# Kernel tuning notes

Hardware: AMD Instinct MI355X
Metric: run time of the kernel (lower is better)

## Reference

```python
import jax, jax.numpy as jnp
import numpy as np

EPS = 1e-5  # torch InstanceNorm2d default eps

def conv1x1(x, w, b):
    # x: [B,C,H,W], w: [O,C], b: [O]
    return jnp.einsum('bchw,oc->bohw', x, w) + b[None, :, None, None]

def instance_norm(x):
    # InstanceNorm2d(affine=False): normalize per-sample, per-channel over H,W
    mean = jnp.mean(x, axis=(2, 3), keepdims=True)
    var = jnp.var(x, axis=(2, 3), keepdims=True)
    return (x - mean) * jax.lax.rsqrt(var + EPS)

def proj(x, w, b):
    return jax.nn.relu(instance_norm(conv1x1(x, w, b)))

def setup_inputs() -> dict:
    key = jax.random.key(0)
    ks = jax.random.split(key, 9)
    B, C, Ci, H, W = 16, 256, 128, 64, 64
    s_in = 1.0 / np.sqrt(C)
    s_mid = 1.0 / np.sqrt(Ci)
    return {
        'x': jax.random.normal(ks[0], (B, C, H, W), jnp.float32),
        'g_w': jax.random.normal(ks[1], (Ci, C), jnp.float32) * s_in,
        'g_b': jax.random.normal(ks[2], (Ci,), jnp.float32) * s_in,
        'theta_w': jax.random.normal(ks[3], (Ci, C), jnp.float32) * s_in,
        'theta_b': jax.random.normal(ks[4], (Ci,), jnp.float32) * s_in,
        'phi_w': jax.random.normal(ks[5], (Ci, C), jnp.float32) * s_in,
        'phi_b': jax.random.normal(ks[6], (Ci,), jnp.float32) * s_in,
        'W_w': jax.random.normal(ks[7], (C, Ci), jnp.float32) * s_mid,
        'W_b': jax.random.normal(ks[8], (C,), jnp.float32) * s_mid,
    }

def reference(x, g_w, g_b, theta_w, theta_b, phi_w, phi_b, W_w, W_b):
    B, C, H, W = x.shape
    Ci = g_w.shape[0]
    N = H * W
    g_x = proj(x, g_w, g_b).reshape(B, Ci, N)        # [B,Ci,N]
    theta_x = proj(x, theta_w, theta_b).reshape(B, Ci, N)
    phi_x = proj(x, phi_w, phi_b).reshape(B, Ci, N)
    # channel-attention Gram matrix [B,Ci,Ci], softmax over last dim
    f = jnp.einsum('bin,bjn->bij', theta_x, phi_x)
    attn = jax.nn.softmax(f, axis=2)
    y = jnp.einsum('bij,bjn->bin', attn, g_x)        # [B,Ci,N]
    # replicate torch permute(0,2,1).contiguous().view(B,Ci,H,W)
    y = jnp.transpose(y, (0, 2, 1)).reshape(B, Ci, H, W)
    y = instance_norm(conv1x1(y, W_w, W_b))
    return y + x
```

## Files before the change

### kernel.cpp

```cpp
#include <hip/hip_runtime.h>

#define DEVINL __device__ __forceinline__

typedef __attribute__((ext_vector_type(8))) _Float16 h8v;
typedef __attribute__((ext_vector_type(4))) float f32x4;
typedef __attribute__((ext_vector_type(8))) unsigned short us8;
typedef __attribute__((ext_vector_type(4))) unsigned short us4;

DEVINL unsigned short f2h(float f) {
  return __builtin_bit_cast(unsigned short, (_Float16)f);
}
DEVINL float h2f(unsigned short u) {
  return (float)__builtin_bit_cast(_Float16, u);
}

__global__ __launch_bounds__(256)
void prep_weights(const float* __restrict__ g_w, const float* __restrict__ th_w,
                  const float* __restrict__ ph_w, const float* __restrict__ W_w,
                  unsigned short* __restrict__ wall_h, unsigned short* __restrict__ wall_l,
                  unsigned short* __restrict__ w2h)
{
  const int i = blockIdx.x * 256 + threadIdx.x;
  float v;
  if (i < 32768) v = th_w[i];
  else if (i < 65536) v = ph_w[i - 32768];
  else v = g_w[i - 65536];
  const unsigned short h = f2h(v);
  wall_h[i] = h;
  if (i < 65536) wall_l[i] = f2h(v - h2f(h));
  if (i < 32768) w2h[i] = f2h(W_w[i]);
}

__global__ __launch_bounds__(512, 2)
void proj_gemm(const unsigned short* __restrict__ wall_h,
               const unsigned short* __restrict__ wall_l,
               const float* __restrict__ x,
               unsigned short* __restrict__ zh, unsigned short* __restrict__ zl,
               float* __restrict__ partials)
{
  __shared__ __align__(16) unsigned short smem[64512];
  unsigned short* As_h = smem;
  unsigned short* As_l = smem + 27648;
  unsigned short* Bs_h = smem + 46080;
  unsigned short* Bs_l = smem + 55296;

  const int t = threadIdx.x;
  const int lane = t & 63;
  const int wave = t >> 6;
  const int wm = wave >> 1, wn = wave & 1;
  const int lr = lane & 15, lk = lane >> 4;
  const int b = blockIdx.z;
  const int bx = blockIdx.x;
  const int nbase = bx * 128;
  const float* xs = x + (long)b * 256 * 4096;

  f32x4 acc[6][4];
#pragma unroll
  for (int i = 0; i < 6; ++i)
#pragma unroll
    for (int j = 0; j < 4; ++j) acc[i][j] = (f32x4)0.0f;

  const int nl = t & 127, cg = t >> 7;

  for (int kt = 0; kt < 4; ++kt) {
    const int k0 = kt * 64;
#pragma unroll
    for (int i = 0; i < 6; ++i) {
      const int q = i * 512 + t;
      const int row = q >> 3, c = q & 7;
      *(us8*)&As_h[row * 72 + c * 8] = *(const us8*)&wall_h[(long)row * 256 + k0 + c * 8];
    }
#pragma unroll
    for (int i = 0; i < 4; ++i) {
      const int q = i * 512 + t;
      const int row = q >> 3, c = q & 7;
      *(us8*)&As_l[row * 72 + c * 8] = *(const us8*)&wall_l[(long)row * 256 + k0 + c * 8];
    }
#pragma unroll
    for (int hp = 0; hp < 2; ++hp) {
      float xv[8];
#pragma unroll
      for (int i = 0; i < 8; ++i)
        xv[i] = xs[(long)(k0 + cg * 16 + hp * 8 + i) * 4096 + nbase + nl];
      us8 h8, l8;
#pragma unroll
      for (int e = 0; e < 8; ++e) {
        const unsigned short hb = f2h(xv[e]);
        h8[e] = hb;
        l8[e] = f2h(xv[e] - h2f(hb));
      }
      *(us8*)&Bs_h[nl * 72 + cg * 16 + hp * 8] = h8;
      *(us8*)&Bs_l[nl * 72 + cg * 16 + hp * 8] = l8;
    }
    __syncthreads();

#pragma unroll
    for (int ks = 0; ks < 2; ++ks) {
      const int ko = ks * 32 + lk * 8;
      h8v bh[4], bl[4];
#pragma unroll
      for (int ni = 0; ni < 4; ++ni) {
        const int r = (wn * 64 + ni * 16 + lr) * 72 + ko;
        bh[ni] = *(const h8v*)&Bs_h[r];
        bl[ni] = *(const h8v*)&Bs_l[r];
      }
#pragma unroll
      for (int mi = 0; mi < 6; ++mi) {
        const int fr = mi * 4 + wm;
        const h8v ah = *(const h8v*)&As_h[(fr * 16 + lr) * 72 + ko];
        if (fr < 16) {
          const h8v al = *(const h8v*)&As_l[(fr * 16 + lr) * 72 + ko];
#pragma unroll
          for (int ni = 0; ni < 4; ++ni) {
            acc[mi][ni] = __builtin_amdgcn_mfma_f32_16x16x32_f16(bh[ni], ah, acc[mi][ni], 0, 0, 0);
            acc[mi][ni] = __builtin_amdgcn_mfma_f32_16x16x32_f16(bl[ni], ah, acc[mi][ni], 0, 0, 0);
            acc[mi][ni] = __builtin_amdgcn_mfma_f32_16x16x32_f16(bh[ni], al, acc[mi][ni], 0, 0, 0);
          }
        } else {
#pragma unroll
          for (int ni = 0; ni < 4; ++ni)
            acc[mi][ni] = __builtin_amdgcn_mfma_f32_16x16x32_f16(bh[ni], ah, acc[mi][ni], 0, 0, 0);
        }
      }
    }
    __syncthreads();
  }

  float* sbuf = (float*)smem;
  unsigned short* T = smem + 12288;
#pragma unroll
  for (int mi = 0; mi < 6; ++mi) {
    float s = 0.f, ss = 0.f;
#pragma unroll
    for (int ni = 0; ni < 4; ++ni)
#pragma unroll
      for (int r = 0; r < 4; ++r) {
        const float v = acc[mi][ni][r];
        s += v; ss += v * v;
      }
    const int fr = mi * 4 + wm;
    const int slot = ((fr * 16 + lr) * 8 + (wn * 4 + lk)) * 2;
    sbuf[slot] = s; sbuf[slot + 1] = ss;
  }
  __syncthreads();
  if (t < 384) {
    float s = 0.f, ss = 0.f;
#pragma unroll
    for (int w = 0; w < 8; ++w) {
      s += sbuf[(t * 8 + w) * 2];
      ss += sbuf[(t * 8 + w) * 2 + 1];
    }
    const long pidx = ((long)bx * 6144 + b * 384 + t) * 2;
    partials[pidx] = s; partials[pidx + 1] = ss;
  }
#pragma unroll
  for (int mi = 0; mi < 6; ++mi)
#pragma unroll
    for (int ni = 0; ni < 4; ++ni) {
      const int gm = (mi * 4 + wm) * 16 + lr;
      const int gn = wn * 64 + ni * 16 + lk * 4;
      us4 hv;
#pragma unroll
      for (int r = 0; r < 4; ++r) hv[r] = f2h(acc[mi][ni][r]);
      *(us4*)&T[gm * 132 + gn] = hv;
    }
  __syncthreads();
#pragma unroll
  for (int i = 0; i < 12; ++i) {
    const int q = i * 512 + t;
    const int row = q >> 4, c = q & 15;
    const us8 v = *(const us8*)&T[row * 132 + c * 8];
    *(us8*)&zh[((long)b * 384 + row) * 4096 + nbase + c * 8] = v;
  }
  __syncthreads();
#pragma unroll
  for (int mi = 0; mi < 4; ++mi)
#pragma unroll
    for (int ni = 0; ni < 4; ++ni) {
      const int gm = (mi * 4 + wm) * 16 + lr;
      const int gn = wn * 64 + ni * 16 + lk * 4;
      us4 lv;
#pragma unroll
      for (int r = 0; r < 4; ++r) {
        const float v = acc[mi][ni][r];
        lv[r] = f2h(v - h2f(f2h(v)));
      }
      *(us4*)&T[gm * 132 + gn] = lv;
    }
  __syncthreads();
#pragma unroll
  for (int i = 0; i < 8; ++i) {
    const int q = i * 512 + t;
    const int row = q >> 4, c = q & 15;
    const us8 v = *(const us8*)&T[row * 132 + c * 8];
    *(us8*)&zl[((long)b * 256 + row) * 4096 + nbase + c * 8] = v;
  }
}

__global__ __launch_bounds__(256)
void stats_reduce(const float* __restrict__ partials, float* __restrict__ stats)
{
  const int row = blockIdx.x * 256 + threadIdx.x;
  float s = 0.f, ss = 0.f;
#pragma unroll
  for (int k = 0; k < 32; ++k) {
    s += partials[((long)k * 6144 + row) * 2];
    ss += partials[((long)k * 6144 + row) * 2 + 1];
  }
  const float mean = s * (1.f / 4096.f);
  const float var = ss * (1.f / 4096.f) - mean * mean;
  const float rs = rsqrtf(fmaxf(var, 0.f) + 1e-5f);
  stats[row * 2] = rs;
  stats[row * 2 + 1] = -mean * rs;
}

__global__ __launch_bounds__(256, 2)
void fgemm_norm(const unsigned short* __restrict__ zh, const unsigned short* __restrict__ zl,
                const float* __restrict__ stats, float* __restrict__ fpart)
{
  __shared__ __align__(16) unsigned short As_h[128 * 72];
  __shared__ __align__(16) unsigned short As_l[128 * 72];
  __shared__ __align__(16) unsigned short Bs_h[128 * 72];
  __shared__ __align__(16) unsigned short Bs_l[128 * 72];

  const int t = threadIdx.x;
  const int lane = t & 63;
  const int wave = t >> 6;
  const int wm = wave >> 1, wn = wave & 1;
  const int lr = lane & 15, lk = lane >> 4;
  const int zb = blockIdx.z >> 5, z1 = blockIdx.z & 31;
  const int koff = z1 * 128;

  f32x4 acc[4][4];
#pragma unroll
  for (int i = 0; i < 4; ++i)
#pragma unroll
    for (int j = 0; j < 4; ++j) acc[i][j] = (f32x4)0.0f;

  for (int kt = 0; kt < 2; ++kt) {
    const int k0 = koff + kt * 64;
#pragma unroll
    for (int i = 0; i < 4; ++i) {
      const int q = i * 256 + t;
      const int row = q >> 3, c = q & 7;
#pragma unroll
      for (int op = 0; op < 2; ++op) {
        const int zrow = op * 128 + row;
        const us8 h = *(const us8*)&zh[((long)zb * 384 + zrow) * 4096 + k0 + c * 8];
        const us8 l = *(const us8*)&zl[((long)zb * 256 + zrow) * 4096 + k0 + c * 8];
        const int srow = zb * 384 + zrow;
        const float rs = stats[srow * 2];
        const float nmrs = stats[srow * 2 + 1];
        us8 oh, ol;
#pragma unroll
        for (int e = 0; e < 8; ++e) {
          const float v = h2f(h[e]) + h2f(l[e]);
          const float nv = fmaxf(__builtin_fmaf(v, rs, nmrs), 0.f);
          const unsigned short hb = f2h(nv);
          oh[e] = hb;
          ol[e] = f2h(nv - h2f(hb));
        }
        unsigned short* dh = op ? Bs_h : As_h;
        unsigned short* dl = op ? Bs_l : As_l;
        *(us8*)&dh[row * 72 + c * 8] = oh;
        *(us8*)&dl[row * 72 + c * 8] = ol;
      }
    }
    __syncthreads();
#pragma unroll
    for (int ks = 0; ks < 2; ++ks) {
      const int ko = ks * 32 + lk * 8;
      h8v ah[4], bh[4], al[4], bl[4];
#pragma unroll
      for (int mi = 0; mi < 4; ++mi) {
        const int r = (wm * 64 + mi * 16 + lr) * 72 + ko;
        ah[mi] = *(const h8v*)&As_h[r];
        al[mi] = *(const h8v*)&As_l[r];
      }
#pragma unroll
      for (int ni = 0; ni < 4; ++ni) {
        const int r = (wn * 64 + ni * 16 + lr) * 72 + ko;
        bh[ni] = *(const h8v*)&Bs_h[r];
        bl[ni] = *(const h8v*)&Bs_l[r];
      }
#pragma unroll
      for (int mi = 0; mi < 4; ++mi)
#pragma unroll
        for (int ni = 0; ni < 4; ++ni) {
          acc[mi][ni] = __builtin_amdgcn_mfma_f32_16x16x32_f16(bh[ni], ah[mi], acc[mi][ni], 0, 0, 0);
          acc[mi][ni] = __builtin_amdgcn_mfma_f32_16x16x32_f16(bl[ni], ah[mi], acc[mi][ni], 0, 0, 0);
          acc[mi][ni] = __builtin_amdgcn_mfma_f32_16x16x32_f16(bh[ni], al[mi], acc[mi][ni], 0, 0, 0);
        }
    }
    __syncthreads();
  }

  const long cOff = ((long)zb * 32 + z1) * 16384;
#pragma unroll
  for (int mi = 0; mi < 4; ++mi)
#pragma unroll
    for (int ni = 0; ni < 4; ++ni) {
      const int gm = wm * 64 + mi * 16 + lr;
      const int gn = wn * 64 + ni * 16 + lk * 4;
      *(f32x4*)&fpart[cOff + (long)gm * 128 + gn] = acc[mi][ni];
    }
}

__global__ __launch_bounds__(256, 2)
void gemm_y(const unsigned short* __restrict__ Ah0, const unsigned short* __restrict__ Bh0,
            unsigned short* __restrict__ Cout,
            int lda, int ldb, int ldc, int ksteps, int z1count,
            long aS1, long aS2, long bS1, long bS2, long cS1, long cS2)
{
  __shared__ __align__(16) unsigned short smem[18432];
  unsigned short* As = smem;
  unsigned short* Bs = smem + 9216;

  const int t = threadIdx.x;
  const int lane = t & 63;
  const int wave = t >> 6;
  const int wm = wave >> 1, wn = wave & 1;
  const int lr = lane & 15, lk = lane >> 4;

  const int z = blockIdx.z;
  const int zb = z / z1count, z1 = z - zb * z1count;
  const unsigned short* Ah = Ah0 + zb * aS2 + z1 * aS1;
  const unsigned short* Bh = Bh0 + zb * bS2 + z1 * bS1;
  const long cOff = zb * cS2 + z1 * cS1;

  f32x4 acc[4][4];
#pragma unroll
  for (int i = 0; i < 4; ++i)
#pragma unroll
    for (int j = 0; j < 4; ++j) acc[i][j] = (f32x4)0.0f;

  for (int kt = 0; kt < ksteps; ++kt) {
    const int k0 = kt * 64;
#pragma unroll
    for (int i = 0; i < 4; ++i) {
      const int q = i * 256 + t;
      const int row = q >> 3, c = q & 7;
      const int lo = row * 72 + c * 8;
      *(us8*)&As[lo] = *(const us8*)&Ah[(long)row * lda + k0 + c * 8];
      *(us8*)&Bs[lo] = *(const us8*)&Bh[(long)row * ldb + k0 + c * 8];
    }
    __syncthreads();
#pragma unroll
    for (int ks = 0; ks < 2; ++ks) {
      const int ko = ks * 32 + lk * 8;
      h8v ah[4], bh[4];
#pragma unroll
      for (int mi = 0; mi < 4; ++mi)
        ah[mi] = *(const h8v*)&As[(wm * 64 + mi * 16 + lr) * 72 + ko];
#pragma unroll
      for (int ni = 0; ni < 4; ++ni)
        bh[ni] = *(const h8v*)&Bs[(wn * 64 + ni * 16 + lr) * 72 + ko];
#pragma unroll
      for (int mi = 0; mi < 4; ++mi)
#pragma unroll
        for (int ni = 0; ni < 4; ++ni)
          acc[mi][ni] = __builtin_amdgcn_mfma_f32_16x16x32_f16(bh[ni], ah[mi], acc[mi][ni], 0, 0, 0);
    }
    __syncthreads();
  }

  unsigned short* T = smem;
#pragma unroll
  for (int mi = 0; mi < 4; ++mi)
#pragma unroll
    for (int ni = 0; ni < 4; ++ni) {
      const int gm = wm * 64 + mi * 16 + lr;
      const int gn = wn * 64 + ni * 16 + lk * 4;
      us4 o;
#pragma unroll
      for (int r = 0; r < 4; ++r) o[r] = f2h(acc[mi][ni][r]);
      *(us4*)&T[gm * 132 + gn] = o;
    }
  __syncthreads();
#pragma unroll
  for (int i = 0; i < 8; ++i) {
    const int q = i * 256 + t;
    const int row = q >> 4, c = q & 15;
    const us8 v = *(const us8*)&T[row * 132 + c * 8];
    *(us8*)&Cout[cOff + (long)row * ldc + c * 8] = v;
  }
}

__global__ __launch_bounds__(256, 2)
void conv2_gemm(const unsigned short* __restrict__ w2h,
                const unsigned short* __restrict__ y4T,
                unsigned short* __restrict__ z2b)
{
  __shared__ __align__(16) unsigned short smem[33792];
  unsigned short* As = smem;
  unsigned short* Bs = smem + 18432;

  const int t = threadIdx.x;
  const int lane = t & 63;
  const int wave = t >> 6;
  const int wm = wave >> 1, wn = wave & 1;
  const int lr = lane & 15, lk = lane >> 4;
  const int b = blockIdx.z;
  const int nbase = blockIdx.x * 128;
  const unsigned short* Bh = y4T + (long)b * 4096 * 128 + (long)nbase * 128;

  f32x4 acc[8][4];
#pragma unroll
  for (int i = 0; i < 8; ++i)
#pragma unroll
    for (int j = 0; j < 4; ++j) acc[i][j] = (f32x4)0.0f;

  for (int kt = 0; kt < 2; ++kt) {
    const int k0 = kt * 64;
#pragma unroll
    for (int i = 0; i < 8; ++i) {
      const int q = i * 256 + t;
      const int row = q >> 3, c = q & 7;
      *(us8*)&As[row * 72 + c * 8] = *(const us8*)&w2h[(long)row * 128 + k0 + c * 8];
    }
#pragma unroll
    for (int i = 0; i < 4; ++i) {
      const int q = i * 256 + t;
      const int row = q >> 3, c = q & 7;
      *(us8*)&Bs[row * 72 + c * 8] = *(const us8*)&Bh[(long)row * 128 + k0 + c * 8];
    }
    __syncthreads();
#pragma unroll
    for (int ks = 0; ks < 2; ++ks) {
      const int ko = ks * 32 + lk * 8;
      h8v ah[8], bh[4];
#pragma unroll
      for (int mi = 0; mi < 8; ++mi)
        ah[mi] = *(const h8v*)&As[(wm * 128 + mi * 16 + lr) * 72 + ko];
#pragma unroll
      for (int ni = 0; ni < 4; ++ni)
        bh[ni] = *(const h8v*)&Bs[(wn * 64 + ni * 16 + lr) * 72 + ko];
#pragma unroll
      for (int mi = 0; mi < 8; ++mi)
#pragma unroll
        for (int ni = 0; ni < 4; ++ni)
          acc[mi][ni] = __builtin_amdgcn_mfma_f32_16x16x32_f16(bh[ni], ah[mi], acc[mi][ni], 0, 0, 0);
    }
    __syncthreads();
  }

  unsigned short* T = smem;
#pragma unroll
  for (int mi = 0; mi < 8; ++mi)
#pragma unroll
    for (int ni = 0; ni < 4; ++ni) {
      const int gm = wm * 128 + mi * 16 + lr;
      const int gn = wn * 64 + ni * 16 + lk * 4;
      us4 o;
#pragma unroll
      for (int r = 0; r < 4; ++r) o[r] = f2h(acc[mi][ni][r]);
      *(us4*)&T[gm * 132 + gn] = o;
    }
  __syncthreads();
#pragma unroll
  for (int i = 0; i < 16; ++i) {
    const int q = i * 256 + t;
    const int row = q >> 4, c = q & 15;
    const us8 v = *(const us8*)&T[row * 132 + c * 8];
    *(us8*)&z2b[((long)b * 256 + row) * 4096 + nbase + c * 8] = v;
  }
}

__global__ __launch_bounds__(256)
void norm_transpose_g(const unsigned short* __restrict__ zh,
                      const float* __restrict__ stats,
                      unsigned short* __restrict__ gT)
{
  __shared__ unsigned short T[64 * 136];
  const int b = blockIdx.y, n0 = blockIdx.x * 64;
  const int t = threadIdx.x;
  const int c = t >> 1, part = t & 1;
  const int grow = b * 384 + 256 + c;
  const float rs = stats[grow * 2];
  const float nmrs = stats[grow * 2 + 1];
  const long off = (long)grow * 4096 + n0 + part * 32;
#pragma unroll
  for (int j = 0; j < 4; ++j) {
    const us8 h = *(const us8*)&zh[off + j * 8];
#pragma unroll
    for (int e = 0; e < 8; ++e) {
      const float nv = fmaxf(__builtin_fmaf(h2f(h[e]), rs, nmrs), 0.f);
      T[(part * 32 + j * 8 + e) * 136 + c] = f2h(nv);
    }
  }
  __syncthreads();
  const int nl = t >> 2, q = t & 3;
  const long obase = ((long)b * 4096 + n0 + nl) * 128 + q * 32;
#pragma unroll
  for (int k = 0; k < 4; ++k) {
    us8 o;
#pragma unroll
    for (int e = 0; e < 8; ++e) o[e] = T[nl * 136 + q * 32 + k * 8 + e];
    *(us8*)&gT[obase + k * 8] = o;
  }
}

__global__ __launch_bounds__(64)
void softmax_attn(const float* __restrict__ fpart, unsigned short* __restrict__ attn)
{
  const int row = blockIdx.x;
  const int b = row >> 7, i = row & 127;
  const int t = threadIdx.x;
  float v0 = 0.f, v1 = 0.f;
#pragma unroll
  for (int kc = 0; kc < 32; ++kc) {
    const float* p = fpart + ((long)(b * 32 + kc)) * 16384 + i * 128;
    v0 += p[t];
    v1 += p[t + 64];
  }
  float mx = fmaxf(v0, v1);
  for (int o = 32; o > 0; o >>= 1) mx = fmaxf(mx, __shfl_xor(mx, o));
  const float e0 = __expf(v0 - mx), e1 = __expf(v1 - mx);
  float s = e0 + e1;
  for (int o = 32; o > 0; o >>= 1) s += __shfl_xor(s, o);
  const float inv = 1.f / s;
  attn[(long)row * 128 + t] = f2h(e0 * inv);
  attn[(long)row * 128 + t + 64] = f2h(e1 * inv);
}

__global__ __launch_bounds__(256)
void finalize(const unsigned short* __restrict__ z2b, const float* __restrict__ x,
              float* __restrict__ out)
{
  const int row = blockIdx.x;
  const long base = (long)row * 4096;
  const int t = threadIdx.x;
  float v[16];
  float s = 0.f, ss = 0.f;
#pragma unroll
  for (int h = 0; h < 2; ++h) {
    us8 u = *(const us8*)&z2b[base + t * 16 + h * 8];
#pragma unroll
    for (int e = 0; e < 8; ++e) {
      const float f = h2f(u[e]);
      v[h * 8 + e] = f;
      s += f; ss += f * f;
    }
  }
  __shared__ float r0[256], r1[256];
  r0[t] = s; r1[t] = ss;
  __syncthreads();
  for (int o = 128; o > 0; o >>= 1) {
    if (t < o) { r0[t] += r0[t + o]; r1[t] += r1[t + o]; }
    __syncthreads();
  }
  const float mean = r0[0] * (1.f / 4096.f);
  const float var = r1[0] * (1.f / 4096.f) - mean * mean;
  const float rs = rsqrtf(fmaxf(var, 0.f) + 1e-5f);
#pragma unroll
  for (int i = 0; i < 4; ++i) {
    f32x4 xr = *(const f32x4*)&x[base + t * 16 + i * 4];
    f32x4 o;
#pragma unroll
    for (int e = 0; e < 4; ++e) o[e] = (v[i * 4 + e] - mean) * rs + xr[e];
    *(f32x4*)&out[base + t * 16 + i * 4] = o;
  }
}

extern "C" void kernel_launch(void* const* d_in, const int* in_sizes, int n_in,
                              void* d_out, int out_size, void* d_ws, size_t ws_size,
                              hipStream_t stream)
{
  const float* x    = (const float*)d_in[0];
  const float* g_w  = (const float*)d_in[1];
  const float* th_w = (const float*)d_in[3];
  const float* ph_w = (const float*)d_in[5];
  const float* W_w  = (const float*)d_in[7];

  char* ws = (char*)d_ws;
  const size_t MB = 1024ull * 1024ull;
  if (ws_size < 186 * MB) return;

  unsigned short* zh       = (unsigned short*)(ws);
  unsigned short* zl       = (unsigned short*)(ws + 51 * MB);
  float*          fpart    = (float*)(ws + 85 * MB);
  unsigned short* attn     = (unsigned short*)(ws + 119 * MB);
  unsigned short* gT       = (unsigned short*)(ws + 120 * MB);
  unsigned short* y4T      = (unsigned short*)(ws + 137 * MB);
  unsigned short* z2b      = (unsigned short*)(ws);
  float*          partials = (float*)(ws + 154 * MB);
  float*          stats    = (float*)(ws + 158 * MB);
  unsigned short* wall_h   = (unsigned short*)(ws + 159 * MB);
  unsigned short* wall_l   = (unsigned short*)(ws + 159 * MB + 256 * 1024);
  unsigned short* w2h      = (unsigned short*)(ws + 159 * MB + 512 * 1024);

  prep_weights<<<dim3(384), 256, 0, stream>>>(g_w, th_w, ph_w, W_w, wall_h, wall_l, w2h);

  proj_gemm<<<dim3(32, 1, 16), 512, 0, stream>>>(wall_h, wall_l, x, zh, zl, partials);

  stats_reduce<<<dim3(24), 256, 0, stream>>>(partials, stats);

  norm_transpose_g<<<dim3(64, 16), 256, 0, stream>>>(zh, stats, gT);

  fgemm_norm<<<dim3(1, 1, 512), 256, 0, stream>>>(zh, zl, stats, fpart);

  softmax_attn<<<dim3(2048), 64, 0, stream>>>(fpart, attn);

  gemm_y<<<dim3(1, 1, 512), 256, 0, stream>>>(
      attn, gT, y4T,
      128, 4096, 128, 2, 32,
      0, 16384, 128, (long)4096 * 128, 16384, (long)4096 * 128);

  conv2_gemm<<<dim3(32, 1, 16), 256, 0, stream>>>(w2h, y4T, z2b);

  finalize<<<dim3(4096), 256, 0, stream>>>(z2b, x, (float*)d_out);
}
```

Before: 154.5 us.

## Split projection GEMM into split-fp16 and plain-fp16 kernels with smaller tiles

The single 512-thread projection kernel, which handled all 384 output rows per block, is split into two templated launches. One computes theta/phi with the three-MFMA hi/lo split over 128-row tiles across two y-blocks. The other computes g with plain fp16 and skips all lo-part loads and conversions. This cuts LDS use per block and gives more, smaller blocks for better occupancy and load balance, at the cost of re-reading and re-converting x three times plus an extra launch. The LDS transpose stride also changes from 132 to 136, which changes the bank-conflict pattern.

```diff
diff --git a/kernel.cpp b/kernel.cpp
--- a/kernel.cpp
+++ b/kernel.cpp
@@ -31,18 +31,19 @@
   if (i < 32768) w2h[i] = f2h(W_w[i]);
 }
 
-__global__ __launch_bounds__(512, 2)
+template<bool THREE>
+__global__ __launch_bounds__(256, 2)
 void proj_gemm(const unsigned short* __restrict__ wall_h,
                const unsigned short* __restrict__ wall_l,
                const float* __restrict__ x,
                unsigned short* __restrict__ zh, unsigned short* __restrict__ zl,
                float* __restrict__ partials)
 {
-  __shared__ __align__(16) unsigned short smem[64512];
+  __shared__ __align__(16) unsigned short smem[THREE ? 36864 : 18432];
   unsigned short* As_h = smem;
-  unsigned short* As_l = smem + 27648;
-  unsigned short* Bs_h = smem + 46080;
-  unsigned short* Bs_l = smem + 55296;
+  unsigned short* Bs_h = smem + 9216;
+  unsigned short* As_l = THREE ? smem + 18432 : nullptr;
+  unsigned short* Bs_l = THREE ? smem + 27648 : nullptr;
 
   const int t = threadIdx.x;
   const int lane = t & 63;
@@ -52,11 +53,12 @@
   const int b = blockIdx.z;
   const int bx = blockIdx.x;
   const int nbase = bx * 128;
+  const int rowbase = THREE ? blockIdx.y * 128 : 256;
   const float* xs = x + (long)b * 256 * 4096;
 
-  f32x4 acc[6][4];
-#pragma unroll
-  for (int i = 0; i < 6; ++i)
+  f32x4 acc[4][4];
+#pragma unroll
+  for (int i = 0; i < 4; ++i)
 #pragma unroll
     for (int j = 0; j < 4; ++j) acc[i][j] = (f32x4)0.0f;
 
@@ -65,32 +67,28 @@
   for (int kt = 0; kt < 4; ++kt) {
     const int k0 = kt * 64;
 #pragma unroll
-    for (int i = 0; i < 6; ++i) {
-      const int q = i * 512 + t;
+    for (int i = 0; i < 4; ++i) {
+      const int q = i * 256 + t;
       const int row = q >> 3, c = q & 7;
-      *(us8*)&As_h[row * 72 + c * 8] = *(const us8*)&wall_h[(long)row * 256 + k0 + c * 8];
-    }
-#pragma unroll
-    for (int i = 0; i < 4; ++i) {
-      const int q = i * 512 + t;
-      const int row = q >> 3, c = q & 7;
-      *(us8*)&As_l[row * 72 + c * 8] = *(const us8*)&wall_l[(long)row * 256 + k0 + c * 8];
-    }
-#pragma unroll
-    for (int hp = 0; hp < 2; ++hp) {
+      *(us8*)&As_h[row * 72 + c * 8] = *(const us8*)&wall_h[(long)(rowbase + row) * 256 + k0 + c * 8];
+      if (THREE)
+        *(us8*)&As_l[row * 72 + c * 8] = *(const us8*)&wall_l[(long)(rowbase + row) * 256 + k0 + c * 8];
+    }
+#pragma unroll
+    for (int hp = 0; hp < 4; ++hp) {
       float xv[8];
 #pragma unroll
       for (int i = 0; i < 8; ++i)
-        xv[i] = xs[(long)(k0 + cg * 16 + hp * 8 + i) * 4096 + nbase + nl];
+        xv[i] = xs[(long)(k0 + cg * 32 + hp * 8 + i) * 4096 + nbase + nl];
       us8 h8, l8;
 #pragma unroll
       for (int e = 0; e < 8; ++e) {
         const unsigned short hb = f2h(xv[e]);
         h8[e] = hb;
-        l8[e] = f2h(xv[e] - h2f(hb));
-      }
-      *(us8*)&Bs_h[nl * 72 + cg * 16 + hp * 8] = h8;
-      *(us8*)&Bs_l[nl * 72 + cg * 16 + hp * 8] = l8;
+        if (THREE) l8[e] = f2h(xv[e] - h2f(hb));
+      }
+      *(us8*)&Bs_h[nl * 72 + cg * 32 + hp * 8] = h8;
+      if (THREE) *(us8*)&Bs_l[nl * 72 + cg * 32 + hp * 8] = l8;
     }
     __syncthreads();
 
@@ -102,14 +100,14 @@
       for (int ni = 0; ni < 4; ++ni) {
         const int r = (wn * 64 + ni * 16 + lr) * 72 + ko;
         bh[ni] = *(const h8v*)&Bs_h[r];
-        bl[ni] = *(const h8v*)&Bs_l[r];
-      }
-#pragma unroll
-      for (int mi = 0; mi < 6; ++mi) {
-        const int fr = mi * 4 + wm;
-        const h8v ah = *(const h8v*)&As_h[(fr * 16 + lr) * 72 + ko];
-        if (fr < 16) {
-          const h8v al = *(const h8v*)&As_l[(fr * 16 + lr) * 72 + ko];
+        if (THREE) bl[ni] = *(const h8v*)&Bs_l[r];
+      }
+#pragma unroll
+      for (int mi = 0; mi < 4; ++mi) {
+        const int r = (wm * 64 + mi * 16 + lr) * 72 + ko;
+        const h8v ah = *(const h8v*)&As_h[r];
+        if (THREE) {
+          const h8v al = *(const h8v*)&As_l[r];
 #pragma unroll
           for (int ni = 0; ni < 4; ++ni) {
             acc[mi][ni] = __builtin_amdgcn_mfma_f32_16x16x32_f16(bh[ni], ah, acc[mi][ni], 0, 0, 0);
@@ -127,9 +125,8 @@
   }
 
   float* sbuf = (float*)smem;
-  unsigned short* T = smem + 12288;
-#pragma unroll
-  for (int mi = 0; mi < 6; ++mi) {
+#pragma unroll
+  for (int mi = 0; mi < 4; ++mi) {
     float s = 0.f, ss = 0.f;
 #pragma unroll
     for (int ni = 0; ni < 4; ++ni)
@@ -138,62 +135,67 @@
         const float v = acc[mi][ni][r];
         s += v; ss += v * v;
       }
-    const int fr = mi * 4 + wm;
-    const int slot = ((fr * 16 + lr) * 8 + (wn * 4 + lk)) * 2;
+    const int row = wm * 64 + mi * 16 + lr;
+    const int slot = (row * 8 + (wn * 4 + lk)) * 2;
     sbuf[slot] = s; sbuf[slot + 1] = ss;
   }
   __syncthreads();
-  if (t < 384) {
+  if (t < 128) {
     float s = 0.f, ss = 0.f;
 #pragma unroll
     for (int w = 0; w < 8; ++w) {
       s += sbuf[(t * 8 + w) * 2];
       ss += sbuf[(t * 8 + w) * 2 + 1];
     }
-    const long pidx = ((long)bx * 6144 + b * 384 + t) * 2;
+    const long pidx = ((long)bx * 6144 + b * 384 + rowbase + t) * 2;
     partials[pidx] = s; partials[pidx + 1] = ss;
   }
-#pragma unroll
-  for (int mi = 0; mi < 6; ++mi)
+  __syncthreads();
+
+  unsigned short* T = smem;
+#pragma unroll
+  for (int mi = 0; mi < 4; ++mi)
 #pragma unroll
     for (int ni = 0; ni < 4; ++ni) {
-      const int gm = (mi * 4 + wm) * 16 + lr;
+      const int gm = wm * 64 + mi * 16 + lr;
       const int gn = wn * 64 + ni * 16 + lk * 4;
       us4 hv;
 #pragma unroll
       for (int r = 0; r < 4; ++r) hv[r] = f2h(acc[mi][ni][r]);
-      *(us4*)&T[gm * 132 + gn] = hv;
+      *(us4*)&T[gm * 136 + gn] = hv;
     }
   __syncthreads();
 #pragma unroll
-  for (int i = 0; i < 12; ++i) {
-    const int q = i * 512 + t;
+  for (int i = 0; i < 8; ++i) {
+    const int q = i * 256 + t;
     const int row = q >> 4, c = q & 15;
-    const us8 v = *(const us8*)&T[row * 132 + c * 8];
-    *(us8*)&zh[((long)b * 384 + row) * 4096 + nbase + c * 8] = v;
-  }
-  __syncthreads();
-#pragma unroll
-  for (int mi = 0; mi < 4; ++mi)
-#pragma unroll
-    for (int ni = 0; ni < 4; ++ni) {
-      const int gm = (mi * 4 + wm) * 16 + lr;
-      const int gn = wn * 64 + ni * 16 + lk * 4;
-      us4 lv;
-#pragma unroll
-      for (int r = 0; r < 4; ++r) {
-        const float v = acc[mi][ni][r];
-        lv[r] = f2h(v - h2f(f2h(v)));
-      }
-      *(us4*)&T[gm * 132 + gn] = lv;
-    }
-  __syncthreads();
-#pragma unroll
-  for (int i = 0; i < 8; ++i) {
-    const int q = i * 512 + t;
-    const int row = q >> 4, c = q & 15;
-    const us8 v = *(const us8*)&T[row * 132 + c * 8];
-    *(us8*)&zl[((long)b * 256 + row) * 4096 + nbase + c * 8] = v;
+    const us8 v = *(const us8*)&T[row * 136 + c * 8];
+    *(us8*)&zh[((long)b * 384 + rowbase + row) * 4096 + nbase + c * 8] = v;
+  }
+  if (THREE) {
+    __syncthreads();
+#pragma unroll
+    for (int mi = 0; mi < 4; ++mi)
+#pragma unroll
+      for (int ni = 0; ni < 4; ++ni) {
+        const int gm = wm * 64 + mi * 16 + lr;
+        const int gn = wn * 64 + ni * 16 + lk * 4;
+        us4 lv;
+#pragma unroll
+        for (int r = 0; r < 4; ++r) {
+          const float v = acc[mi][ni][r];
+          lv[r] = f2h(v - h2f(f2h(v)));
+        }
+        *(us4*)&T[gm * 136 + gn] = lv;
+      }
+    __syncthreads();
+#pragma unroll
+    for (int i = 0; i < 8; ++i) {
+      const int q = i * 256 + t;
+      const int row = q >> 4, c = q & 15;
+      const us8 v = *(const us8*)&T[row * 136 + c * 8];
+      *(us8*)&zl[((long)b * 256 + rowbase + row) * 4096 + nbase + c * 8] = v;
+    }
   }
 }
 
@@ -374,14 +376,14 @@
       us4 o;
 #pragma unroll
       for (int r = 0; r < 4; ++r) o[r] = f2h(acc[mi][ni][r]);
-      *(us4*)&T[gm * 132 + gn] = o;
+      *(us4*)&T[gm * 136 + gn] = o;
     }
   __syncthreads();
 #pragma unroll
   for (int i = 0; i < 8; ++i) {
     const int q = i * 256 + t;
     const int row = q >> 4, c = q & 15;
-    const us8 v = *(const us8*)&T[row * 132 + c * 8];
+    const us8 v = *(const us8*)&T[row * 136 + c * 8];
     *(us8*)&Cout[cOff + (long)row * ldc + c * 8] = v;
   }
 }
@@ -391,7 +393,7 @@
                 const unsigned short* __restrict__ y4T,
                 unsigned short* __restrict__ z2b)
 {
-  __shared__ __align__(16) unsigned short smem[33792];
+  __shared__ __align__(16) unsigned short smem[35072];
   unsigned short* As = smem;
   unsigned short* Bs = smem + 18432;
 
@@ -454,14 +456,14 @@
       us4 o;
 #pragma unroll
       for (int r = 0; r < 4; ++r) o[r] = f2h(acc[mi][ni][r]);
-      *(us4*)&T[gm * 132 + gn] = o;
+      *(us4*)&T[gm * 136 + gn] = o;
     }
   __syncthreads();
 #pragma unroll
   for (int i = 0; i < 16; ++i) {
     const int q = i * 256 + t;
     const int row = q >> 4, c = q & 15;
-    const us8 v = *(const us8*)&T[row * 132 + c * 8];
+    const us8 v = *(const us8*)&T[row * 136 + c * 8];
     *(us8*)&z2b[((long)b * 256 + row) * 4096 + nbase + c * 8] = v;
   }
 }
@@ -591,7 +593,8 @@
 
   prep_weights<<<dim3(384), 256, 0, stream>>>(g_w, th_w, ph_w, W_w, wall_h, wall_l, w2h);
 
-  proj_gemm<<<dim3(32, 1, 16), 512, 0, stream>>>(wall_h, wall_l, x, zh, zl, partials);
+  proj_gemm<true><<<dim3(32, 2, 16), 256, 0, stream>>>(wall_h, wall_l, x, zh, zl, partials);
+  proj_gemm<false><<<dim3(32, 1, 16), 256, 0, stream>>>(wall_h, nullptr, x, zh, nullptr, partials);
 
   stats_reduce<<<dim3(24), 256, 0, stream>>>(partials, stats);
 
```

Measured after the change: 160.2 us. +3.7%, slower.

## Double-buffer x tile in proj_gemm and pack softmax rows four per block

Applied to the files above, without the earlier changes.

The projection GEMM now prefetches the next K-slice of x into registers while the MFMAs for the current slice run, and writes it into a double-buffered B tile in LDS. The B row stride is also changed from 72 to 68. The goal is to hide global load latency behind compute, at the cost of more LDS (about 158 KB for the block) and more register pressure. Separately, softmax_attn now handles four rows per 256-thread block instead of one row per 64-thread block, and conv2_gemm's shared buffer grows slightly.

```diff
diff --git a/kernel.cpp b/kernel.cpp
--- a/kernel.cpp
+++ b/kernel.cpp
@@ -38,11 +38,11 @@
                unsigned short* __restrict__ zh, unsigned short* __restrict__ zl,
                float* __restrict__ partials)
 {
-  __shared__ __align__(16) unsigned short smem[64512];
+  __shared__ __align__(16) unsigned short smem[80896];
   unsigned short* As_h = smem;
   unsigned short* As_l = smem + 27648;
   unsigned short* Bs_h = smem + 46080;
-  unsigned short* Bs_l = smem + 55296;
+  unsigned short* Bs_l = smem + 63488;
 
   const int t = threadIdx.x;
   const int lane = t & 63;
@@ -62,47 +62,59 @@
 
   const int nl = t & 127, cg = t >> 7;
 
-  for (int kt = 0; kt < 4; ++kt) {
-    const int k0 = kt * 64;
+  {
 #pragma unroll
     for (int i = 0; i < 6; ++i) {
       const int q = i * 512 + t;
       const int row = q >> 3, c = q & 7;
-      *(us8*)&As_h[row * 72 + c * 8] = *(const us8*)&wall_h[(long)row * 256 + k0 + c * 8];
+      *(us8*)&As_h[row * 72 + c * 8] = *(const us8*)&wall_h[(long)row * 256 + c * 8];
     }
 #pragma unroll
     for (int i = 0; i < 4; ++i) {
       const int q = i * 512 + t;
       const int row = q >> 3, c = q & 7;
-      *(us8*)&As_l[row * 72 + c * 8] = *(const us8*)&wall_l[(long)row * 256 + k0 + c * 8];
-    }
+      *(us8*)&As_l[row * 72 + c * 8] = *(const us8*)&wall_l[(long)row * 256 + c * 8];
+    }
+    float xv[16];
+#pragma unroll
+    for (int i = 0; i < 16; ++i)
+      xv[i] = xs[(long)(cg * 16 + i) * 4096 + nbase + nl];
 #pragma unroll
     for (int hp = 0; hp < 2; ++hp) {
-      float xv[8];
-#pragma unroll
-      for (int i = 0; i < 8; ++i)
-        xv[i] = xs[(long)(k0 + cg * 16 + hp * 8 + i) * 4096 + nbase + nl];
       us8 h8, l8;
 #pragma unroll
       for (int e = 0; e < 8; ++e) {
-        const unsigned short hb = f2h(xv[e]);
+        const float v = xv[hp * 8 + e];
+        const unsigned short hb = f2h(v);
         h8[e] = hb;
-        l8[e] = f2h(xv[e] - h2f(hb));
-      }
-      *(us8*)&Bs_h[nl * 72 + cg * 16 + hp * 8] = h8;
-      *(us8*)&Bs_l[nl * 72 + cg * 16 + hp * 8] = l8;
-    }
-    __syncthreads();
-
+        l8[e] = f2h(v - h2f(hb));
+      }
+      *(us8*)&Bs_h[nl * 68 + cg * 16 + hp * 8] = h8;
+      *(us8*)&Bs_l[nl * 68 + cg * 16 + hp * 8] = l8;
+    }
+    __syncthreads();
+  }
+
+  for (int kt = 0; kt < 4; ++kt) {
+    const int cur = (kt & 1) * 8704;
+    float xv[16];
+    if (kt < 3) {
+      const int kn = (kt + 1) * 64;
+#pragma unroll
+      for (int i = 0; i < 16; ++i)
+        xv[i] = xs[(long)(kn + cg * 16 + i) * 4096 + nbase + nl];
+    }
+    const unsigned short* Bh = Bs_h + cur;
+    const unsigned short* Bl = Bs_l + cur;
 #pragma unroll
     for (int ks = 0; ks < 2; ++ks) {
       const int ko = ks * 32 + lk * 8;
       h8v bh[4], bl[4];
 #pragma unroll
       for (int ni = 0; ni < 4; ++ni) {
-        const int r = (wn * 64 + ni * 16 + lr) * 72 + ko;
-        bh[ni] = *(const h8v*)&Bs_h[r];
-        bl[ni] = *(const h8v*)&Bs_l[r];
+        const int r = (wn * 64 + ni * 16 + lr) * 68 + ko;
+        bh[ni] = *(const h8v*)&Bh[r];
+        bl[ni] = *(const h8v*)&Bl[r];
       }
 #pragma unroll
       for (int mi = 0; mi < 6; ++mi) {
@@ -124,6 +136,36 @@
       }
     }
     __syncthreads();
+    if (kt < 3) {
+      const int kn = (kt + 1) * 64;
+#pragma unroll
+      for (int i = 0; i < 6; ++i) {
+        const int q = i * 512 + t;
+        const int row = q >> 3, c = q & 7;
+        *(us8*)&As_h[row * 72 + c * 8] = *(const us8*)&wall_h[(long)row * 256 + kn + c * 8];
+      }
+#pragma unroll
+      for (int i = 0; i < 4; ++i) {
+        const int q = i * 512 + t;
+        const int row = q >> 3, c = q & 7;
+        *(us8*)&As_l[row * 72 + c * 8] = *(const us8*)&wall_l[(long)row * 256 + kn + c * 8];
+      }
+      const int nxt = ((kt + 1) & 1) * 8704;
+#pragma unroll
+      for (int hp = 0; hp < 2; ++hp) {
+        us8 h8, l8;
+#pragma unroll
+        for (int e = 0; e < 8; ++e) {
+          const float v = xv[hp * 8 + e];
+          const unsigned short hb = f2h(v);
+          h8[e] = hb;
+          l8[e] = f2h(v - h2f(hb));
+        }
+        *(us8*)&Bs_h[nxt + nl * 68 + cg * 16 + hp * 8] = h8;
+        *(us8*)&Bs_l[nxt + nl * 68 + cg * 16 + hp * 8] = l8;
+      }
+      __syncthreads();
+    }
   }
 
   float* sbuf = (float*)smem;
@@ -391,7 +433,7 @@
                 const unsigned short* __restrict__ y4T,
                 unsigned short* __restrict__ z2b)
 {
-  __shared__ __align__(16) unsigned short smem[33792];
+  __shared__ __align__(16) unsigned short smem[35072];
   unsigned short* As = smem;
   unsigned short* Bs = smem + 18432;
 
@@ -500,12 +542,12 @@
   }
 }
 
-__global__ __launch_bounds__(64)
+__global__ __launch_bounds__(256)
 void softmax_attn(const float* __restrict__ fpart, unsigned short* __restrict__ attn)
 {
-  const int row = blockIdx.x;
+  const int row = blockIdx.x * 4 + (threadIdx.x >> 6);
   const int b = row >> 7, i = row & 127;
-  const int t = threadIdx.x;
+  const int t = threadIdx.x & 63;
   float v0 = 0.f, v1 = 0.f;
 #pragma unroll
   for (int kc = 0; kc < 32; ++kc) {
@@ -599,7 +641,7 @@
 
   fgemm_norm<<<dim3(1, 1, 512), 256, 0, stream>>>(zh, zl, stats, fpart);
 
-  softmax_attn<<<dim3(2048), 64, 0, stream>>>(fpart, attn);
+  softmax_attn<<<dim3(512), 256, 0, stream>>>(fpart, attn);
 
   gemm_y<<<dim3(1, 1, 512), 256, 0, stream>>>(
       attn, gT, y4T,
```

Result: slower. 184.3 us (+19.3%).

## Store theta/phi projections as fp32 directly, retile conv2 and batch softmax rows

Applied to the files above, without the earlier changes.

proj_gemm now writes the theta/phi accumulators straight to global memory as fp32 and the g rows as fp16, dropping the hi/lo fp16 split and the shared-memory staging transpose with its barriers. fgemm_norm reads the fp32 values directly instead of recombining two fp16 halves. conv2_gemm is retiled to 64-column blocks with a four-wave M split, doubling the grid and lowering register and LDS use. softmax packs four rows per 256-thread block. The direct fragment stores are less coalesced than the staged stores and trade the same byte count for fewer passes.

```diff
diff --git a/kernel.cpp b/kernel.cpp
--- a/kernel.cpp
+++ b/kernel.cpp
@@ -35,7 +35,7 @@
 void proj_gemm(const unsigned short* __restrict__ wall_h,
                const unsigned short* __restrict__ wall_l,
                const float* __restrict__ x,
-               unsigned short* __restrict__ zh, unsigned short* __restrict__ zl,
+               float* __restrict__ zr, unsigned short* __restrict__ zg,
                float* __restrict__ partials)
 {
   __shared__ __align__(16) unsigned short smem[64512];
@@ -127,7 +127,6 @@
   }
 
   float* sbuf = (float*)smem;
-  unsigned short* T = smem + 12288;
 #pragma unroll
   for (int mi = 0; mi < 6; ++mi) {
     float s = 0.f, ss = 0.f;
@@ -153,48 +152,22 @@
     const long pidx = ((long)bx * 6144 + b * 384 + t) * 2;
     partials[pidx] = s; partials[pidx + 1] = ss;
   }
+
 #pragma unroll
   for (int mi = 0; mi < 6; ++mi)
 #pragma unroll
     for (int ni = 0; ni < 4; ++ni) {
       const int gm = (mi * 4 + wm) * 16 + lr;
-      const int gn = wn * 64 + ni * 16 + lk * 4;
-      us4 hv;
-#pragma unroll
-      for (int r = 0; r < 4; ++r) hv[r] = f2h(acc[mi][ni][r]);
-      *(us4*)&T[gm * 132 + gn] = hv;
-    }
-  __syncthreads();
-#pragma unroll
-  for (int i = 0; i < 12; ++i) {
-    const int q = i * 512 + t;
-    const int row = q >> 4, c = q & 15;
-    const us8 v = *(const us8*)&T[row * 132 + c * 8];
-    *(us8*)&zh[((long)b * 384 + row) * 4096 + nbase + c * 8] = v;
-  }
-  __syncthreads();
-#pragma unroll
-  for (int mi = 0; mi < 4; ++mi)
-#pragma unroll
-    for (int ni = 0; ni < 4; ++ni) {
-      const int gm = (mi * 4 + wm) * 16 + lr;
-      const int gn = wn * 64 + ni * 16 + lk * 4;
-      us4 lv;
-#pragma unroll
-      for (int r = 0; r < 4; ++r) {
-        const float v = acc[mi][ni][r];
-        lv[r] = f2h(v - h2f(f2h(v)));
-      }
-      *(us4*)&T[gm * 132 + gn] = lv;
-    }
-  __syncthreads();
-#pragma unroll
-  for (int i = 0; i < 8; ++i) {
-    const int q = i * 512 + t;
-    const int row = q >> 4, c = q & 15;
-    const us8 v = *(const us8*)&T[row * 132 + c * 8];
-    *(us8*)&zl[((long)b * 256 + row) * 4096 + nbase + c * 8] = v;
-  }
+      const int gn = nbase + wn * 64 + ni * 16 + lk * 4;
+      if (mi < 4) {
+        *(f32x4*)&zr[((long)b * 256 + gm) * 4096 + gn] = acc[mi][ni];
+      } else {
+        us4 hv;
+#pragma unroll
+        for (int r = 0; r < 4; ++r) hv[r] = f2h(acc[mi][ni][r]);
+        *(us4*)&zg[((long)b * 128 + (gm - 256)) * 4096 + gn] = hv;
+      }
+    }
 }
 
 __global__ __launch_bounds__(256)
@@ -215,7 +188,7 @@
 }
 
 __global__ __launch_bounds__(256, 2)
-void fgemm_norm(const unsigned short* __restrict__ zh, const unsigned short* __restrict__ zl,
+void fgemm_norm(const float* __restrict__ zr,
                 const float* __restrict__ stats, float* __restrict__ fpart)
 {
   __shared__ __align__(16) unsigned short As_h[128 * 72];
@@ -246,15 +219,16 @@
 #pragma unroll
       for (int op = 0; op < 2; ++op) {
         const int zrow = op * 128 + row;
-        const us8 h = *(const us8*)&zh[((long)zb * 384 + zrow) * 4096 + k0 + c * 8];
-        const us8 l = *(const us8*)&zl[((long)zb * 256 + zrow) * 4096 + k0 + c * 8];
+        const float* src = zr + ((long)zb * 256 + zrow) * 4096 + k0 + c * 8;
+        const f32x4 v0 = *(const f32x4*)&src[0];
+        const f32x4 v1 = *(const f32x4*)&src[4];
         const int srow = zb * 384 + zrow;
         const float rs = stats[srow * 2];
         const float nmrs = stats[srow * 2 + 1];
         us8 oh, ol;
 #pragma unroll
         for (int e = 0; e < 8; ++e) {
-          const float v = h2f(h[e]) + h2f(l[e]);
+          const float v = (e < 4) ? v0[e] : v1[e - 4];
           const float nv = fmaxf(__builtin_fmaf(v, rs, nmrs), 0.f);
           const unsigned short hb = f2h(nv);
           oh[e] = hb;
@@ -391,22 +365,22 @@
                 const unsigned short* __restrict__ y4T,
                 unsigned short* __restrict__ z2b)
 {
-  __shared__ __align__(16) unsigned short smem[33792];
+  __shared__ __align__(16) unsigned short smem[23040];
   unsigned short* As = smem;
   unsigned short* Bs = smem + 18432;
 
   const int t = threadIdx.x;
   const int lane = t & 63;
   const int wave = t >> 6;
-  const int wm = wave >> 1, wn = wave & 1;
+  const int wm = wave;
   const int lr = lane & 15, lk = lane >> 4;
   const int b = blockIdx.z;
-  const int nbase = blockIdx.x * 128;
+  const int nbase = blockIdx.x * 64;
   const unsigned short* Bh = y4T + (long)b * 4096 * 128 + (long)nbase * 128;
 
-  f32x4 acc[8][4];
-#pragma unroll
-  for (int i = 0; i < 8; ++i)
+  f32x4 acc[4][4];
+#pragma unroll
+  for (int i = 0; i < 4; ++i)
 #pragma unroll
     for (int j = 0; j < 4; ++j) acc[i][j] = (f32x4)0.0f;
 
@@ -419,7 +393,7 @@
       *(us8*)&As[row * 72 + c * 8] = *(const us8*)&w2h[(long)row * 128 + k0 + c * 8];
     }
 #pragma unroll
-    for (int i = 0; i < 4; ++i) {
+    for (int i = 0; i < 2; ++i) {
       const int q = i * 256 + t;
       const int row = q >> 3, c = q & 7;
       *(us8*)&Bs[row * 72 + c * 8] = *(const us8*)&Bh[(long)row * 128 + k0 + c * 8];
@@ -428,15 +402,15 @@
 #pragma unroll
     for (int ks = 0; ks < 2; ++ks) {
       const int ko = ks * 32 + lk * 8;
-      h8v ah[8], bh[4];
-#pragma unroll
-      for (int mi = 0; mi < 8; ++mi)
-        ah[mi] = *(const h8v*)&As[(wm * 128 + mi * 16 + lr) * 72 + ko];
+      h8v ah[4], bh[4];
+#pragma unroll
+      for (int mi = 0; mi < 4; ++mi)
+        ah[mi] = *(const h8v*)&As[(wm * 64 + mi * 16 + lr) * 72 + ko];
 #pragma unroll
       for (int ni = 0; ni < 4; ++ni)
-        bh[ni] = *(const h8v*)&Bs[(wn * 64 + ni * 16 + lr) * 72 + ko];
-#pragma unroll
-      for (int mi = 0; mi < 8; ++mi)
+        bh[ni] = *(const h8v*)&Bs[(ni * 16 + lr) * 72 + ko];
+#pragma unroll
+      for (int mi = 0; mi < 4; ++mi)
 #pragma unroll
         for (int ni = 0; ni < 4; ++ni)
           acc[mi][ni] = __builtin_amdgcn_mfma_f32_16x16x32_f16(bh[ni], ah[mi], acc[mi][ni], 0, 0, 0);
@@ -446,28 +420,28 @@
 
   unsigned short* T = smem;
 #pragma unroll
-  for (int mi = 0; mi < 8; ++mi)
+  for (int mi = 0; mi < 4; ++mi)
 #pragma unroll
     for (int ni = 0; ni < 4; ++ni) {
-      const int gm = wm * 128 + mi * 16 + lr;
-      const int gn = wn * 64 + ni * 16 + lk * 4;
+      const int gm = wm * 64 + mi * 16 + lr;
+      const int gn = ni * 16 + lk * 4;
       us4 o;
 #pragma unroll
       for (int r = 0; r < 4; ++r) o[r] = f2h(acc[mi][ni][r]);
-      *(us4*)&T[gm * 132 + gn] = o;
+      *(us4*)&T[gm * 72 + gn] = o;
     }
   __syncthreads();
 #pragma unroll
-  for (int i = 0; i < 16; ++i) {
+  for (int i = 0; i < 8; ++i) {
     const int q = i * 256 + t;
-    const int row = q >> 4, c = q & 15;
-    const us8 v = *(const us8*)&T[row * 132 + c * 8];
+    const int row = q >> 3, c = q & 7;
+    const us8 v = *(const us8*)&T[row * 72 + c * 8];
     *(us8*)&z2b[((long)b * 256 + row) * 4096 + nbase + c * 8] = v;
   }
 }
 
 __global__ __launch_bounds__(256)
-void norm_transpose_g(const unsigned short* __restrict__ zh,
+void norm_transpose_g(const unsigned short* __restrict__ zg,
                       const float* __restrict__ stats,
                       unsigned short* __restrict__ gT)
 {
@@ -478,10 +452,10 @@
   const int grow = b * 384 + 256 + c;
   const float rs = stats[grow * 2];
   const float nmrs = stats[grow * 2 + 1];
-  const long off = (long)grow * 4096 + n0 + part * 32;
+  const long off = ((long)b * 128 + c) * 4096 + n0 + part * 32;
 #pragma unroll
   for (int j = 0; j < 4; ++j) {
-    const us8 h = *(const us8*)&zh[off + j * 8];
+    const us8 h = *(const us8*)&zg[off + j * 8];
 #pragma unroll
     for (int e = 0; e < 8; ++e) {
       const float nv = fmaxf(__builtin_fmaf(h2f(h[e]), rs, nmrs), 0.f);
@@ -500,12 +474,12 @@
   }
 }
 
-__global__ __launch_bounds__(64)
+__global__ __launch_bounds__(256)
 void softmax_attn(const float* __restrict__ fpart, unsigned short* __restrict__ attn)
 {
-  const int row = blockIdx.x;
+  const int row = blockIdx.x * 4 + (threadIdx.x >> 6);
   const int b = row >> 7, i = row & 127;
-  const int t = threadIdx.x;
+  const int t = threadIdx.x & 63;
   float v0 = 0.f, v1 = 0.f;
 #pragma unroll
   for (int kc = 0; kc < 32; ++kc) {
@@ -576,37 +550,37 @@
   const size_t MB = 1024ull * 1024ull;
   if (ws_size < 186 * MB) return;
 
-  unsigned short* zh       = (unsigned short*)(ws);
-  unsigned short* zl       = (unsigned short*)(ws + 51 * MB);
-  float*          fpart    = (float*)(ws + 85 * MB);
-  unsigned short* attn     = (unsigned short*)(ws + 119 * MB);
-  unsigned short* gT       = (unsigned short*)(ws + 120 * MB);
-  unsigned short* y4T      = (unsigned short*)(ws + 137 * MB);
+  float*          zr       = (float*)(ws);
+  unsigned short* zg       = (unsigned short*)(ws + 64 * MB);
+  float*          fpart    = (float*)(ws + 80 * MB);
+  unsigned short* attn     = (unsigned short*)(ws + 112 * MB);
+  unsigned short* gT       = (unsigned short*)(ws + 113 * MB);
+  unsigned short* y4T      = (unsigned short*)(ws + 129 * MB);
   unsigned short* z2b      = (unsigned short*)(ws);
-  float*          partials = (float*)(ws + 154 * MB);
-  float*          stats    = (float*)(ws + 158 * MB);
-  unsigned short* wall_h   = (unsigned short*)(ws + 159 * MB);
-  unsigned short* wall_l   = (unsigned short*)(ws + 159 * MB + 256 * 1024);
-  unsigned short* w2h      = (unsigned short*)(ws + 159 * MB + 512 * 1024);
+  float*          partials = (float*)(ws + 145 * MB);
+  float*          stats    = (float*)(ws + 149 * MB);
+  unsigned short* wall_h   = (unsigned short*)(ws + 150 * MB);
+  unsigned short* wall_l   = (unsigned short*)(ws + 150 * MB + 256 * 1024);
+  unsigned short* w2h      = (unsigned short*)(ws + 150 * MB + 512 * 1024);
 
   prep_weights<<<dim3(384), 256, 0, stream>>>(g_w, th_w, ph_w, W_w, wall_h, wall_l, w2h);
 
-  proj_gemm<<<dim3(32, 1, 16), 512, 0, stream>>>(wall_h, wall_l, x, zh, zl, partials);
+  proj_gemm<<<dim3(32, 1, 16), 512, 0, stream>>>(wall_h, wall_l, x, zr, zg, partials);
 
   stats_reduce<<<dim3(24), 256, 0, stream>>>(partials, stats);
 
-  norm_transpose_g<<<dim3(64, 16), 256, 0, stream>>>(zh, stats, gT);
-
-  fgemm_norm<<<dim3(1, 1, 512), 256, 0, stream>>>(zh, zl, stats, fpart);
-
-  softmax_attn<<<dim3(2048), 64, 0, stream>>>(fpart, attn);
+  norm_transpose_g<<<dim3(64, 16), 256, 0, stream>>>(zg, stats, gT);
+
+  fgemm_norm<<<dim3(1, 1, 512), 256, 0, stream>>>(zr, stats, fpart);
+
+  softmax_attn<<<dim3(512), 256, 0, stream>>>(fpart, attn);
 
   gemm_y<<<dim3(1, 1, 512), 256, 0, stream>>>(
       attn, gT, y4T,
       128, 4096, 128, 2, 32,
       0, 16384, 128, (long)4096 * 128, 16384, (long)4096 * 128);
 
-  conv2_gemm<<<dim3(32, 1, 16), 256, 0, stream>>>(w2h, y4T, z2b);
+  conv2_gemm<<<dim3(64, 1, 16), 256, 0, stream>>>(w2h, y4T, z2b);
 
   finalize<<<dim3(4096), 256, 0, stream>>>(z2b, x, (float*)d_out);
 }
```

Measured after the change: 148.4 us. 3.9% less time.
